# Performance work log

Measured on AMD Instinct MI355X. Metric: run time of the kernel, lower is better.

The kernel has to match this reference:

```python
import jax, jax.numpy as jnp
import numpy as np

F = 256  # filters
FQ = F // 8  # query/key channels


def setup_inputs() -> dict:
    key = jax.random.key(0)
    ks = jax.random.split(key, 9)
    B, H, W = 4, 64, 64
    s_in = 1.0 / np.sqrt(F)
    inp = {
        "inputs": jax.random.normal(ks[0], (B, H, W, F), jnp.float32),
        "Wq": jax.random.normal(ks[1], (F, FQ), jnp.float32) * s_in,
        "bq": jnp.zeros((FQ,), jnp.float32),
        "Wk": jax.random.normal(ks[2], (F, FQ), jnp.float32) * s_in,
        "bk": jnp.zeros((FQ,), jnp.float32),
        "Wv": jax.random.normal(ks[3], (F, F), jnp.float32) * s_in,
        "bv": jnp.zeros((F,), jnp.float32),
        "Wo": jax.random.normal(ks[4], (F, F), jnp.float32) * s_in,
        "bo": jnp.zeros((F,), jnp.float32),
    }
    return inp


def reference(inputs, Wq, bq, Wk, bk, Wv, bv, Wo, bo):
    B, H, W, C = inputs.shape
    N = H * W
    x = inputs.reshape(B, N, C)  # 1x1 conv == per-token linear
    q = jax.nn.relu(jnp.einsum('bnc,cd->bnd', x, Wq) + bq)  # [B,N,FQ]
    k = jax.nn.relu(jnp.einsum('bnc,cd->bnd', x, Wk) + bk)  # [B,N,FQ]
    v = jax.nn.relu(jnp.einsum('bnc,cd->bnd', x, Wv) + bv)  # [B,N,C]
    # unscaled full attention (as in the original module)
    attn = jax.nn.softmax(jnp.einsum('bnd,bmd->bnm', q, k), axis=-1)  # [B,N,N]
    attended = jnp.einsum('bnm,bmc->bnc', attn, v)  # [B,N,C]
    out = jax.nn.relu(jnp.einsum('bnc,cd->bnd', attended, Wo) + bo)
    return inputs + out.reshape(B, H, W, C)
```

## Files before the change

kernel.cpp:

```cpp
#include <hip/hip_runtime.h>

typedef __attribute__((ext_vector_type(8))) short short8;
typedef __attribute__((ext_vector_type(4))) float floatx4;

#define MFMA16(a, b, c) __builtin_amdgcn_mfma_f32_16x16x32_bf16((a), (b), (c), 0, 0, 0)

#define LDP 72
#define LDO 264
#define LOG2E 1.4426950408889634f
#define PSHIFT 23.083120654223414f

__device__ __forceinline__ float bf2f(unsigned short u) {
  return __uint_as_float(((unsigned int)u) << 16);
}
__device__ __forceinline__ unsigned short f2bf(float f) {
  unsigned int x = __float_as_uint(f);
  x += 0x7FFFu + ((x >> 16) & 1u);
  return (unsigned short)(x >> 16);
}
__device__ __forceinline__ float ld_in(const void* p, long i, int isf32) {
  if (isf32) return ((const float*)p)[i];
  return bf2f(((const unsigned short*)p)[i]);
}
__device__ __forceinline__ short8 ld16(const unsigned short* p) {
  return *(const short8*)__builtin_assume_aligned(p, 16);
}
__device__ __forceinline__ void st16(unsigned short* p, short8 v) {
  *(short8*)__builtin_assume_aligned(p, 16) = v;
}
__device__ __forceinline__ int detect_bad(const unsigned short* x, int idx) {
  const short8 v = ld16(x + (long)idx * 8);
  int bad = 0;
#pragma unroll
  for (int j = 0; j < 8; j++) {
    const unsigned int e = (((unsigned short)v[j]) >> 7) & 0xFFu;
    if (e >= 141u) bad = 1;
  }
  return bad;
}


__global__ __launch_bounds__(256)
void proj_kernel(const void* __restrict__ x,
                 const void* __restrict__ Wq, const void* __restrict__ bq,
                 const void* __restrict__ Wk, const void* __restrict__ bk,
                 const void* __restrict__ Wv, const void* __restrict__ bv,
                 const void* __restrict__ Wo,
                 unsigned short* __restrict__ Qf, unsigned short* __restrict__ Kf,
                 unsigned short* __restrict__ Vf, unsigned short* __restrict__ Wf_o) {
  __shared__ unsigned short Wl[64][LDO];
  __shared__ unsigned short Vl[64][LDP];
  __shared__ int flagl[4];
  const int t = (int)threadIdx.x;
  const int wave = t >> 6, lane = t & 63, quad = lane >> 4, l15 = lane & 15;

  {
    const int bad = detect_bad((const unsigned short*)x, t) |
                    detect_bad((const unsigned short*)x, 256 + t);
    if (lane == 0) flagl[wave] = (__ballot(bad) != 0ull) ? 1 : 0;
  }
  __syncthreads();
  const int isf32 = flagl[0] | flagl[1] | flagl[2] | flagl[3];

  const int blk = (int)blockIdx.x;
  if (blk >= 1280) {
    const int b2 = blk - 1280;
    const int g0 = (b2 >> 2) * 64, c0 = (b2 & 3) * 64;
    const int j = t & 63, r4 = t >> 6;
#pragma unroll
    for (int k2 = 0; k2 < 16; k2++) {
      const int rr = r4 * 16 + k2;
      Vl[j][rr] = f2bf(ld_in(Wo, (long)(c0 + rr) * 256 + g0 + j, isf32));
    }
    __syncthreads();
#pragma unroll
    for (int cc = 0; cc < 2; cc++) {
      const int c = t + cc * 256;
      const int f_l = c >> 6, lane_c = c & 63;
      const int og = f_l >> 1, kse = f_l & 1;
      const int out_l = lane_c & 15, q = lane_c >> 4;
      const short8 v = ld16(&Vl[og * 16 + out_l][kse * 32 + q * 8]);
      st16(Wf_o + (long)(((g0 >> 4) + og) * 8 + (c0 >> 5) + kse) * 512 + lane_c * 8, v);
    }
    return;
  }

  const int ct = blk % 5;
  const long row_base = (long)(blk / 5) * 64;

  if (ct == 0) {
    for (int i = t; i < 16384; i += 256) {
      const int g = i & 63, c = i >> 6;
      const float v = (g < 32) ? ld_in(Wq, (long)c * 32 + g, isf32) * LOG2E
                               : ld_in(Wk, (long)c * 32 + (g - 32), isf32);
      Wl[g][c] = f2bf(v);
    }
  } else {
    const int g0 = (ct - 1) * 64;
    for (int i = t; i < 16384; i += 256) {
      const int j = i & 63, c = i >> 6;
      Wl[j][c] = f2bf(ld_in(Wv, (long)c * 256 + g0 + j, isf32));
    }
  }
  __syncthreads();

  const long arow = row_base + wave * 16 + l15;
  floatx4 acc[4];
  acc[0] = acc[1] = acc[2] = acc[3] = (floatx4)0.0f;

#pragma unroll
  for (int ks = 0; ks < 8; ks++) {
    short8 a;
    if (isf32) {
      const float* xf = (const float*)x + arow * 256 + ks * 32 + quad * 8;
      floatx4 f0 = *(const floatx4*)xf;
      floatx4 f1 = *(const floatx4*)(xf + 4);
#pragma unroll
      for (int j = 0; j < 4; j++) { a[j] = (short)f2bf(f0[j]); a[4 + j] = (short)f2bf(f1[j]); }
    } else {
      a = ld16((const unsigned short*)x + arow * 256 + ks * 32 + quad * 8);
    }
#pragma unroll
    for (int tn = 0; tn < 4; tn++) {
      const short8 bfr = ld16(&Wl[tn * 16 + l15][ks * 32 + quad * 8]);
      acc[tn] = MFMA16(a, bfr, acc[tn]);
    }
  }

  if (ct == 0) {
#pragma unroll
    for (int tn = 0; tn < 4; tn++) {
      const int g = tn * 16 + l15;
      const float bias = (g < 32) ? ld_in(bq, g, isf32) * LOG2E
                                  : ld_in(bk, g - 32, isf32);
#pragma unroll
      for (int r = 0; r < 4; r++)
        Vl[wave * 16 + quad * 4 + r][g] = f2bf(fmaxf(acc[tn][r] + bias, 0.0f));
    }
    __syncthreads();
    const long f0 = row_base >> 4;
#pragma unroll
    for (int cc = 0; cc < 2; cc++) {
      const int c = t + cc * 256;
      const int isK = c >> 8;
      const int c2 = c & 255;
      const int f_l = c2 >> 6, lane_c = c2 & 63;
      const int row_l = lane_c & 15, q = lane_c >> 4;
      const short8 v = ld16(&Vl[f_l * 16 + row_l][isK * 32 + q * 8]);
      unsigned short* dst = isK ? Kf : Qf;
      st16(dst + (f0 + f_l) * 512 + lane_c * 8, v);
    }
  } else {
#pragma unroll
    for (int tn = 0; tn < 4; tn++) {
      const float bias = ld_in(bv, (long)(ct - 1) * 64 + tn * 16 + l15, isf32);
#pragma unroll
      for (int r = 0; r < 4; r++)
        Vl[tn * 16 + l15][wave * 16 + quad * 4 + r] =
            f2bf(fmaxf(acc[tn][r] + bias, 0.0f));
    }
    __syncthreads();
    const long bb = row_base >> 12;
    const int kt = (int)((row_base & 4095) >> 6);
    const long fbase = (bb * 64 + kt) * 32 + (long)(ct - 1) * 8;
#pragma unroll
    for (int cc = 0; cc < 2; cc++) {
      const int c = t * 2 + cc;
      const int f_l = c >> 6, lane_c = c & 63;
      const int cg = f_l >> 1, kh = f_l & 1;
      const int ch_l = lane_c & 15, q = lane_c >> 4;
      const short8 v = ld16(&Vl[cg * 16 + ch_l][kh * 32 + q * 8]);
      st16(Vf + (fbase + f_l) * 512 + lane_c * 8, v);
    }
  }
}

__global__ __launch_bounds__(512, 2)
void flash_kernel(const unsigned short* __restrict__ Qf,
                  const unsigned short* __restrict__ Kf,
                  const unsigned short* __restrict__ Vf,
                  const unsigned short* __restrict__ Wf_o,
                  const void* __restrict__ bo,
                  const void* __restrict__ xin, void* __restrict__ out) {
  __shared__ unsigned short Pl[2][64 * LDP];
  __shared__ unsigned short Ol[64 * LDO];
  __shared__ float Lp[2][64];
  __shared__ float Ll[64];
  __shared__ int flagl[8];

  const int t = (int)threadIdx.x;
  const int wave = t >> 6, lane = t & 63, quad = lane >> 4, l15 = lane & 15;

  {
    const int bad = detect_bad((const unsigned short*)xin, t);
    if (lane == 0) flagl[wave] = (__ballot(bad) != 0ull) ? 1 : 0;
  }

  const int raw = (int)blockIdx.x;
  const int b = raw & 3;
  const int mt = raw >> 2;
  const long qrow0 = (long)b * 4096 + (long)mt * 64;
  const int m = wave & 3, h = wave >> 2;

  const long kfrag0 = (long)b * 256;
  const long vfrag0 = (long)b * 64 * 32;

  const short8 qf = ld16(Qf + ((qrow0 >> 4) + m) * 512 + lane * 8);
  short8 kb[2];
#pragma unroll
  for (int i = 0; i < 2; i++)
    kb[i] = ld16(Kf + (kfrag0 + h * 2 + i) * 512 + lane * 8);

  floatx4 oacc[4][2];
#pragma unroll
  for (int i = 0; i < 4; i++) { oacc[i][0] = (floatx4)0.0f; oacc[i][1] = (floatx4)0.0f; }
  float lpart[4] = {0.0f, 0.0f, 0.0f, 0.0f};

  for (int kt = 0; kt < 64; kt++) {
    short8 vb[2][2];
#pragma unroll
    for (int tv = 0; tv < 2; tv++)
#pragma unroll
      for (int kh = 0; kh < 2; kh++)
        vb[tv][kh] = ld16(Vf + (vfrag0 + (long)kt * 32 + (wave * 2 + tv) * 2 + kh) * 512 + lane * 8);

    floatx4 s[2];
#pragma unroll
    for (int i = 0; i < 2; i++) { s[i] = (floatx4)0.0f; s[i] = MFMA16(qf, kb[i], s[i]); }
    const int ktn = (kt + 1) & 63;
#pragma unroll
    for (int i = 0; i < 2; i++)
      kb[i] = ld16(Kf + (kfrag0 + ktn * 4 + h * 2 + i) * 512 + lane * 8);

    unsigned short* pl = Pl[kt & 1];
#pragma unroll
    for (int i = 0; i < 2; i++)
#pragma unroll
      for (int r = 0; r < 4; r++) {
        const float p = exp2f(s[i][r] - PSHIFT);
        lpart[r] += p;
        pl[(m * 16 + quad * 4 + r) * LDP + h * 32 + i * 16 + l15] = f2bf(p);
      }
    __syncthreads();

    const unsigned short* plr = Pl[kt & 1];
    short8 pa[4][2];
#pragma unroll
    for (int rm = 0; rm < 4; rm++)
#pragma unroll
      for (int kh = 0; kh < 2; kh++)
        pa[rm][kh] = ld16(&plr[(rm * 16 + l15) * LDP + kh * 32 + quad * 8]);

#pragma unroll
    for (int kh = 0; kh < 2; kh++)
#pragma unroll
      for (int tv = 0; tv < 2; tv++)
#pragma unroll
        for (int rm = 0; rm < 4; rm++)
          oacc[rm][tv] = MFMA16(pa[rm][kh], vb[tv][kh], oacc[rm][tv]);
  }

#pragma unroll
  for (int r = 0; r < 4; r++)
#pragma unroll
    for (int off = 1; off < 16; off <<= 1)
      lpart[r] += __shfl_xor(lpart[r], off);
  if (l15 == 0) {
    floatx4 lw;
#pragma unroll
    for (int r = 0; r < 4; r++) lw[r] = lpart[r];
    *(floatx4*)&Lp[h][m * 16 + quad * 4] = lw;
  }
  __syncthreads();
  if (t < 64) Ll[t] = 1.0f / (Lp[0][t] + Lp[1][t]);
  __syncthreads();

#pragma unroll
  for (int rm = 0; rm < 4; rm++) {
    const floatx4 ll = *(const floatx4*)&Ll[rm * 16 + quad * 4];
#pragma unroll
    for (int tv = 0; tv < 2; tv++)
#pragma unroll
      for (int r = 0; r < 4; r++)
        Ol[(rm * 16 + quad * 4 + r) * LDO + wave * 32 + tv * 16 + l15] =
            f2bf(oacc[rm][tv][r] * ll[r]);
  }
  __syncthreads();

  const int isf32 = flagl[0] | flagl[1] | flagl[2] | flagl[3] |
                    flagl[4] | flagl[5] | flagl[6] | flagl[7];
  const int m2 = wave & 3, gh = wave >> 2;
  floatx4 acc2[8];
#pragma unroll
  for (int i = 0; i < 8; i++) acc2[i] = (floatx4)0.0f;
#pragma unroll
  for (int ks = 0; ks < 8; ks++) {
    const short8 a = ld16(&Ol[(m2 * 16 + l15) * LDO + ks * 32 + quad * 8]);
#pragma unroll
    for (int tn = 0; tn < 8; tn++) {
      const short8 bfr = ld16(Wf_o + (long)((gh * 8 + tn) * 8 + ks) * 512 + lane * 8);
      acc2[tn] = MFMA16(a, bfr, acc2[tn]);
    }
  }
  __syncthreads();
#pragma unroll
  for (int tn = 0; tn < 8; tn++) {
    const int g = gh * 128 + tn * 16 + l15;
    const float bias = ld_in(bo, g, isf32);
#pragma unroll
    for (int r = 0; r < 4; r++)
      Ol[(m2 * 16 + quad * 4 + r) * LDO + g] = f2bf(fmaxf(acc2[tn][r] + bias, 0.0f));
  }
  __syncthreads();

  if (isf32) {
    const float* xf = (const float*)xin + qrow0 * 256;
    float* of = (float*)out + qrow0 * 256;
#pragma unroll
    for (int p = 0; p < 8; p++) {
      const int idx = p * 2048 + t * 4;
      const int row = idx >> 8, ch = idx & 255;
      floatx4 xv = *(const floatx4*)(xf + idx);
      floatx4 ov;
#pragma unroll
      for (int j = 0; j < 4; j++) ov[j] = bf2f(Ol[row * LDO + ch + j]) + xv[j];
      *(floatx4*)(of + idx) = ov;
    }
  } else {
    const unsigned short* xh = (const unsigned short*)xin + qrow0 * 256;
    unsigned short* oh = (unsigned short*)out + qrow0 * 256;
#pragma unroll
    for (int p = 0; p < 4; p++) {
      const int idx = p * 4096 + t * 8;
      const int row = idx >> 8, ch = idx & 255;
      const short8 xv = ld16(xh + idx);
      short8 ov;
#pragma unroll
      for (int j = 0; j < 8; j++)
        ov[j] = (short)f2bf(bf2f(Ol[row * LDO + ch + j]) + bf2f((unsigned short)xv[j]));
      st16(oh + idx, ov);
    }
  }
}

extern "C" void kernel_launch(void* const* d_in, const int* in_sizes, int n_in,
                              void* d_out, int out_size, void* d_ws, size_t ws_size,
                              hipStream_t stream) {
  const void* x  = d_in[0];
  const void* Wq = d_in[1]; const void* bq = d_in[2];
  const void* Wk = d_in[3]; const void* bk = d_in[4];
  const void* Wv = d_in[5]; const void* bv = d_in[6];
  const void* Wo = d_in[7]; const void* bo = d_in[8];

  char* ws = (char*)d_ws;
  unsigned short* Qf   = (unsigned short*)ws;
  unsigned short* Kf   = Qf + (long)4 * 4096 * 32;
  unsigned short* Vf   = Kf + (long)4 * 4096 * 32;
  unsigned short* Wf_o = Vf + (long)4 * 256 * 4096;

  proj_kernel<<<1296, 256, 0, stream>>>(x, Wq, bq, Wk, bk, Wv, bv, Wo,
                                        Qf, Kf, Vf, Wf_o);
  flash_kernel<<<256, 512, 0, stream>>>(Qf, Kf, Vf, Wf_o, bo, x, d_out);
}
```

Baseline: 203.4 us.

## Fuse projection and flash attention into one cooperative kernel with grid sync

Merges the projection kernel and the flash-attention kernel into a single cooperative launch of 256 blocks. Each block projects its own 64 rows (Q/K and four V chunks) while holding the input fragments in registers, and the first 16 blocks also repack Wo; a grid-wide sync then separates this phase from attention. The attention loop is unrolled to handle two key tiles per iteration with a larger double-buffered P tile, which halves the barriers. This removes one kernel launch and its gap, in exchange for more LDS per block, a grid-sync cost, every block reloading the full Wv weights, and a projection phase with far fewer blocks than before.

```diff
diff --git a/kernel.cpp b/kernel.cpp
--- a/kernel.cpp
+++ b/kernel.cpp
@@ -1,4 +1,7 @@
 #include <hip/hip_runtime.h>
+#include <hip/hip_cooperative_groups.h>
+
+namespace cg = cooperative_groups;
 
 typedef __attribute__((ext_vector_type(8))) short short8;
 typedef __attribute__((ext_vector_type(4))) float floatx4;
@@ -40,224 +43,212 @@
 }
 
 
-__global__ __launch_bounds__(256)
-void proj_kernel(const void* __restrict__ x,
-                 const void* __restrict__ Wq, const void* __restrict__ bq,
-                 const void* __restrict__ Wk, const void* __restrict__ bk,
-                 const void* __restrict__ Wv, const void* __restrict__ bv,
-                 const void* __restrict__ Wo,
-                 unsigned short* __restrict__ Qf, unsigned short* __restrict__ Kf,
-                 unsigned short* __restrict__ Vf, unsigned short* __restrict__ Wf_o) {
+__global__ __launch_bounds__(512, 2)
+void fused_kernel(const void* __restrict__ x,
+                  const void* __restrict__ Wq, const void* __restrict__ bq,
+                  const void* __restrict__ Wk, const void* __restrict__ bk,
+                  const void* __restrict__ Wv, const void* __restrict__ bv,
+                  const void* __restrict__ Wo, const void* __restrict__ bo,
+                  unsigned short* __restrict__ Qf, unsigned short* __restrict__ Kf,
+                  unsigned short* __restrict__ Vf, unsigned short* __restrict__ Wf_o,
+                  void* __restrict__ out) {
   __shared__ unsigned short Wl[64][LDO];
   __shared__ unsigned short Vl[64][LDP];
-  __shared__ int flagl[4];
+  __shared__ unsigned short Pl[2][2][64 * LDP];
+  __shared__ unsigned short Ol[64 * LDO];
+  __shared__ float Lp[2][64];
+  __shared__ float Ll[64];
+  __shared__ int flagl[8];
+
   const int t = (int)threadIdx.x;
   const int wave = t >> 6, lane = t & 63, quad = lane >> 4, l15 = lane & 15;
 
   {
-    const int bad = detect_bad((const unsigned short*)x, t) |
-                    detect_bad((const unsigned short*)x, 256 + t);
+    const int bad = detect_bad((const unsigned short*)x, t);
     if (lane == 0) flagl[wave] = (__ballot(bad) != 0ull) ? 1 : 0;
   }
   __syncthreads();
-  const int isf32 = flagl[0] | flagl[1] | flagl[2] | flagl[3];
-
-  const int blk = (int)blockIdx.x;
-  if (blk >= 1280) {
-    const int b2 = blk - 1280;
-    const int g0 = (b2 >> 2) * 64, c0 = (b2 & 3) * 64;
-    const int j = t & 63, r4 = t >> 6;
-#pragma unroll
-    for (int k2 = 0; k2 < 16; k2++) {
-      const int rr = r4 * 16 + k2;
-      Vl[j][rr] = f2bf(ld_in(Wo, (long)(c0 + rr) * 256 + g0 + j, isf32));
-    }
-    __syncthreads();
-#pragma unroll
-    for (int cc = 0; cc < 2; cc++) {
-      const int c = t + cc * 256;
-      const int f_l = c >> 6, lane_c = c & 63;
+  const int isf32 = flagl[0] | flagl[1] | flagl[2] | flagl[3] |
+                    flagl[4] | flagl[5] | flagl[6] | flagl[7];
+
+  const int raw = (int)blockIdx.x;
+  const int b = raw & 3;
+  const int mt = raw >> 2;
+  const long row_base = (long)b * 4096 + (long)mt * 64;
+
+  const int pm = wave & 3, ph = wave >> 2;
+  {
+    const long arow = row_base + pm * 16 + l15;
+    short8 a[8];
+#pragma unroll
+    for (int ks = 0; ks < 8; ks++) {
+      if (isf32) {
+        const float* xf = (const float*)x + arow * 256 + ks * 32 + quad * 8;
+        floatx4 f0 = *(const floatx4*)xf;
+        floatx4 f1 = *(const floatx4*)(xf + 4);
+#pragma unroll
+        for (int j = 0; j < 4; j++) { a[ks][j] = (short)f2bf(f0[j]); a[ks][4 + j] = (short)f2bf(f1[j]); }
+      } else {
+        a[ks] = ld16((const unsigned short*)x + arow * 256 + ks * 32 + quad * 8);
+      }
+    }
+
+    for (int chunk = 0; chunk < 5; chunk++) {
+      __syncthreads();
+      if (chunk == 0) {
+        for (int i = t; i < 16384; i += 512) {
+          const int g = i & 63, c = i >> 6;
+          const float v = (g < 32) ? ld_in(Wq, (long)c * 32 + g, isf32) * LOG2E
+                                   : ld_in(Wk, (long)c * 32 + (g - 32), isf32);
+          Wl[g][c] = f2bf(v);
+        }
+      } else {
+        const int g0 = (chunk - 1) * 64;
+        for (int i = t; i < 16384; i += 512) {
+          const int j = i & 63, c = i >> 6;
+          Wl[j][c] = f2bf(ld_in(Wv, (long)c * 256 + g0 + j, isf32));
+        }
+      }
+      __syncthreads();
+
+      floatx4 acc[2];
+      acc[0] = acc[1] = (floatx4)0.0f;
+#pragma unroll
+      for (int ks = 0; ks < 8; ks++)
+#pragma unroll
+        for (int tn = 0; tn < 2; tn++) {
+          const short8 bfr = ld16(&Wl[ph * 32 + tn * 16 + l15][ks * 32 + quad * 8]);
+          acc[tn] = MFMA16(a[ks], bfr, acc[tn]);
+        }
+
+      if (chunk == 0) {
+#pragma unroll
+        for (int tn = 0; tn < 2; tn++) {
+          const int g = ph * 32 + tn * 16 + l15;
+          const float bias = (g < 32) ? ld_in(bq, g, isf32) * LOG2E
+                                      : ld_in(bk, g - 32, isf32);
+#pragma unroll
+          for (int r = 0; r < 4; r++)
+            Vl[pm * 16 + quad * 4 + r][g] = f2bf(fmaxf(acc[tn][r] + bias, 0.0f));
+        }
+        __syncthreads();
+        const int isK = t >> 8, c2 = t & 255;
+        const int f_l = c2 >> 6, lane_c = c2 & 63;
+        const int row_l = lane_c & 15, q = lane_c >> 4;
+        const short8 v = ld16(&Vl[f_l * 16 + row_l][isK * 32 + q * 8]);
+        unsigned short* dst = isK ? Kf : Qf;
+        st16(dst + ((row_base >> 4) + f_l) * 512 + lane_c * 8, v);
+      } else {
+        const int vc = chunk - 1;
+#pragma unroll
+        for (int tn = 0; tn < 2; tn++) {
+          const float bias = ld_in(bv, (long)vc * 64 + ph * 32 + tn * 16 + l15, isf32);
+#pragma unroll
+          for (int r = 0; r < 4; r++)
+            Vl[ph * 32 + tn * 16 + l15][pm * 16 + quad * 4 + r] =
+                f2bf(fmaxf(acc[tn][r] + bias, 0.0f));
+        }
+        __syncthreads();
+        const int f_l = t >> 6, lane_c = t & 63;
+        const int cg2 = f_l >> 1, kh = f_l & 1;
+        const int ch_l = lane_c & 15, q = lane_c >> 4;
+        const short8 v = ld16(&Vl[cg2 * 16 + ch_l][kh * 32 + q * 8]);
+        const long fbase = ((long)b * 64 + mt) * 32 + (long)vc * 8;
+        st16(Vf + (fbase + f_l) * 512 + lane_c * 8, v);
+      }
+    }
+
+    if (raw < 16) {
+      __syncthreads();
+      const int g0 = (raw >> 2) * 64, c0 = (raw & 3) * 64;
+      const int j = t & 63, r8 = t >> 6;
+#pragma unroll
+      for (int k2 = 0; k2 < 8; k2++) {
+        const int rr = r8 * 8 + k2;
+        Vl[j][rr] = f2bf(ld_in(Wo, (long)(c0 + rr) * 256 + g0 + j, isf32));
+      }
+      __syncthreads();
+      const int f_l = t >> 6, lane_c = t & 63;
       const int og = f_l >> 1, kse = f_l & 1;
       const int out_l = lane_c & 15, q = lane_c >> 4;
       const short8 v = ld16(&Vl[og * 16 + out_l][kse * 32 + q * 8]);
       st16(Wf_o + (long)(((g0 >> 4) + og) * 8 + (c0 >> 5) + kse) * 512 + lane_c * 8, v);
     }
-    return;
-  }
-
-  const int ct = blk % 5;
-  const long row_base = (long)(blk / 5) * 64;
-
-  if (ct == 0) {
-    for (int i = t; i < 16384; i += 256) {
-      const int g = i & 63, c = i >> 6;
-      const float v = (g < 32) ? ld_in(Wq, (long)c * 32 + g, isf32) * LOG2E
-                               : ld_in(Wk, (long)c * 32 + (g - 32), isf32);
-      Wl[g][c] = f2bf(v);
-    }
-  } else {
-    const int g0 = (ct - 1) * 64;
-    for (int i = t; i < 16384; i += 256) {
-      const int j = i & 63, c = i >> 6;
-      Wl[j][c] = f2bf(ld_in(Wv, (long)c * 256 + g0 + j, isf32));
-    }
-  }
-  __syncthreads();
-
-  const long arow = row_base + wave * 16 + l15;
-  floatx4 acc[4];
-  acc[0] = acc[1] = acc[2] = acc[3] = (floatx4)0.0f;
-
-#pragma unroll
-  for (int ks = 0; ks < 8; ks++) {
-    short8 a;
-    if (isf32) {
-      const float* xf = (const float*)x + arow * 256 + ks * 32 + quad * 8;
-      floatx4 f0 = *(const floatx4*)xf;
-      floatx4 f1 = *(const floatx4*)(xf + 4);
-#pragma unroll
-      for (int j = 0; j < 4; j++) { a[j] = (short)f2bf(f0[j]); a[4 + j] = (short)f2bf(f1[j]); }
-    } else {
-      a = ld16((const unsigned short*)x + arow * 256 + ks * 32 + quad * 8);
-    }
-#pragma unroll
-    for (int tn = 0; tn < 4; tn++) {
-      const short8 bfr = ld16(&Wl[tn * 16 + l15][ks * 32 + quad * 8]);
-      acc[tn] = MFMA16(a, bfr, acc[tn]);
-    }
-  }
-
-  if (ct == 0) {
-#pragma unroll
-    for (int tn = 0; tn < 4; tn++) {
-      const int g = tn * 16 + l15;
-      const float bias = (g < 32) ? ld_in(bq, g, isf32) * LOG2E
-                                  : ld_in(bk, g - 32, isf32);
-#pragma unroll
-      for (int r = 0; r < 4; r++)
-        Vl[wave * 16 + quad * 4 + r][g] = f2bf(fmaxf(acc[tn][r] + bias, 0.0f));
-    }
-    __syncthreads();
-    const long f0 = row_base >> 4;
-#pragma unroll
-    for (int cc = 0; cc < 2; cc++) {
-      const int c = t + cc * 256;
-      const int isK = c >> 8;
-      const int c2 = c & 255;
-      const int f_l = c2 >> 6, lane_c = c2 & 63;
-      const int row_l = lane_c & 15, q = lane_c >> 4;
-      const short8 v = ld16(&Vl[f_l * 16 + row_l][isK * 32 + q * 8]);
-      unsigned short* dst = isK ? Kf : Qf;
-      st16(dst + (f0 + f_l) * 512 + lane_c * 8, v);
-    }
-  } else {
-#pragma unroll
-    for (int tn = 0; tn < 4; tn++) {
-      const float bias = ld_in(bv, (long)(ct - 1) * 64 + tn * 16 + l15, isf32);
-#pragma unroll
-      for (int r = 0; r < 4; r++)
-        Vl[tn * 16 + l15][wave * 16 + quad * 4 + r] =
-            f2bf(fmaxf(acc[tn][r] + bias, 0.0f));
-    }
-    __syncthreads();
-    const long bb = row_base >> 12;
-    const int kt = (int)((row_base & 4095) >> 6);
-    const long fbase = (bb * 64 + kt) * 32 + (long)(ct - 1) * 8;
-#pragma unroll
-    for (int cc = 0; cc < 2; cc++) {
-      const int c = t * 2 + cc;
-      const int f_l = c >> 6, lane_c = c & 63;
-      const int cg = f_l >> 1, kh = f_l & 1;
-      const int ch_l = lane_c & 15, q = lane_c >> 4;
-      const short8 v = ld16(&Vl[cg * 16 + ch_l][kh * 32 + q * 8]);
-      st16(Vf + (fbase + f_l) * 512 + lane_c * 8, v);
-    }
-  }
-}
-
-__global__ __launch_bounds__(512, 2)
-void flash_kernel(const unsigned short* __restrict__ Qf,
-                  const unsigned short* __restrict__ Kf,
-                  const unsigned short* __restrict__ Vf,
-                  const unsigned short* __restrict__ Wf_o,
-                  const void* __restrict__ bo,
-                  const void* __restrict__ xin, void* __restrict__ out) {
-  __shared__ unsigned short Pl[2][64 * LDP];
-  __shared__ unsigned short Ol[64 * LDO];
-  __shared__ float Lp[2][64];
-  __shared__ float Ll[64];
-  __shared__ int flagl[8];
-
-  const int t = (int)threadIdx.x;
-  const int wave = t >> 6, lane = t & 63, quad = lane >> 4, l15 = lane & 15;
-
-  {
-    const int bad = detect_bad((const unsigned short*)xin, t);
-    if (lane == 0) flagl[wave] = (__ballot(bad) != 0ull) ? 1 : 0;
-  }
-
-  const int raw = (int)blockIdx.x;
-  const int b = raw & 3;
-  const int mt = raw >> 2;
-  const long qrow0 = (long)b * 4096 + (long)mt * 64;
+  }
+
+  cg::this_grid().sync();
+
+  const long qrow0 = row_base;
   const int m = wave & 3, h = wave >> 2;
-
   const long kfrag0 = (long)b * 256;
-  const long vfrag0 = (long)b * 64 * 32;
+  const long vfrag0 = (long)b * 2048;
 
   const short8 qf = ld16(Qf + ((qrow0 >> 4) + m) * 512 + lane * 8);
-  short8 kb[2];
-#pragma unroll
-  for (int i = 0; i < 2; i++)
-    kb[i] = ld16(Kf + (kfrag0 + h * 2 + i) * 512 + lane * 8);
+  short8 kb[2][2];
+#pragma unroll
+  for (int tt = 0; tt < 2; tt++)
+#pragma unroll
+    for (int i = 0; i < 2; i++)
+      kb[tt][i] = ld16(Kf + (kfrag0 + tt * 4 + h * 2 + i) * 512 + lane * 8);
 
   floatx4 oacc[4][2];
 #pragma unroll
   for (int i = 0; i < 4; i++) { oacc[i][0] = (floatx4)0.0f; oacc[i][1] = (floatx4)0.0f; }
   float lpart[4] = {0.0f, 0.0f, 0.0f, 0.0f};
 
-  for (int kt = 0; kt < 64; kt++) {
-    short8 vb[2][2];
-#pragma unroll
-    for (int tv = 0; tv < 2; tv++)
+  for (int it = 0; it < 32; it++) {
+    const int kt0 = it * 2;
+    short8 vb[2][2][2];
+#pragma unroll
+    for (int tt = 0; tt < 2; tt++)
+#pragma unroll
+      for (int tv = 0; tv < 2; tv++)
+#pragma unroll
+        for (int kh = 0; kh < 2; kh++)
+          vb[tt][tv][kh] = ld16(Vf + (vfrag0 + (long)(kt0 + tt) * 32 + (wave * 2 + tv) * 2 + kh) * 512 + lane * 8);
+
+    floatx4 s[2][2];
+#pragma unroll
+    for (int tt = 0; tt < 2; tt++)
+#pragma unroll
+      for (int i = 0; i < 2; i++) { s[tt][i] = (floatx4)0.0f; s[tt][i] = MFMA16(qf, kb[tt][i], s[tt][i]); }
+#pragma unroll
+    for (int tt = 0; tt < 2; tt++)
+#pragma unroll
+      for (int i = 0; i < 2; i++)
+        kb[tt][i] = ld16(Kf + (kfrag0 + (long)((kt0 + 2 + tt) & 63) * 4 + h * 2 + i) * 512 + lane * 8);
+
+#pragma unroll
+    for (int tt = 0; tt < 2; tt++) {
+      unsigned short* pl = Pl[it & 1][tt];
+#pragma unroll
+      for (int i = 0; i < 2; i++)
+#pragma unroll
+        for (int r = 0; r < 4; r++) {
+          const float p = exp2f(s[tt][i][r] - PSHIFT);
+          lpart[r] += p;
+          pl[(m * 16 + quad * 4 + r) * LDP + h * 32 + i * 16 + l15] = f2bf(p);
+        }
+    }
+    __syncthreads();
+
+#pragma unroll
+    for (int tt = 0; tt < 2; tt++) {
+      const unsigned short* plr = Pl[it & 1][tt];
+      short8 pa[4][2];
+#pragma unroll
+      for (int rm = 0; rm < 4; rm++)
+#pragma unroll
+        for (int kh = 0; kh < 2; kh++)
+          pa[rm][kh] = ld16(&plr[(rm * 16 + l15) * LDP + kh * 32 + quad * 8]);
 #pragma unroll
       for (int kh = 0; kh < 2; kh++)
-        vb[tv][kh] = ld16(Vf + (vfrag0 + (long)kt * 32 + (wave * 2 + tv) * 2 + kh) * 512 + lane * 8);
-
-    floatx4 s[2];
-#pragma unroll
-    for (int i = 0; i < 2; i++) { s[i] = (floatx4)0.0f; s[i] = MFMA16(qf, kb[i], s[i]); }
-    const int ktn = (kt + 1) & 63;
-#pragma unroll
-    for (int i = 0; i < 2; i++)
-      kb[i] = ld16(Kf + (kfrag0 + ktn * 4 + h * 2 + i) * 512 + lane * 8);
-
-    unsigned short* pl = Pl[kt & 1];
-#pragma unroll
-    for (int i = 0; i < 2; i++)
-#pragma unroll
-      for (int r = 0; r < 4; r++) {
-        const float p = exp2f(s[i][r] - PSHIFT);
-        lpart[r] += p;
-        pl[(m * 16 + quad * 4 + r) * LDP + h * 32 + i * 16 + l15] = f2bf(p);
-      }
-    __syncthreads();
-
-    const unsigned short* plr = Pl[kt & 1];
-    short8 pa[4][2];
-#pragma unroll
-    for (int rm = 0; rm < 4; rm++)
-#pragma unroll
-      for (int kh = 0; kh < 2; kh++)
-        pa[rm][kh] = ld16(&plr[(rm * 16 + l15) * LDP + kh * 32 + quad * 8]);
-
-#pragma unroll
-    for (int kh = 0; kh < 2; kh++)
-#pragma unroll
-      for (int tv = 0; tv < 2; tv++)
-#pragma unroll
-        for (int rm = 0; rm < 4; rm++)
-          oacc[rm][tv] = MFMA16(pa[rm][kh], vb[tv][kh], oacc[rm][tv]);
+#pragma unroll
+        for (int tv = 0; tv < 2; tv++)
+#pragma unroll
+          for (int rm = 0; rm < 4; rm++)
+            oacc[rm][tv] = MFMA16(pa[rm][kh], vb[tt][tv][kh], oacc[rm][tv]);
+    }
   }
 
 #pragma unroll
@@ -287,8 +278,6 @@
   }
   __syncthreads();
 
-  const int isf32 = flagl[0] | flagl[1] | flagl[2] | flagl[3] |
-                    flagl[4] | flagl[5] | flagl[6] | flagl[7];
   const int m2 = wave & 3, gh = wave >> 2;
   floatx4 acc2[8];
 #pragma unroll
@@ -314,7 +303,7 @@
   __syncthreads();
 
   if (isf32) {
-    const float* xf = (const float*)xin + qrow0 * 256;
+    const float* xf = (const float*)x + qrow0 * 256;
     float* of = (float*)out + qrow0 * 256;
 #pragma unroll
     for (int p = 0; p < 8; p++) {
@@ -327,7 +316,7 @@
       *(floatx4*)(of + idx) = ov;
     }
   } else {
-    const unsigned short* xh = (const unsigned short*)xin + qrow0 * 256;
+    const unsigned short* xh = (const unsigned short*)x + qrow0 * 256;
     unsigned short* oh = (unsigned short*)out + qrow0 * 256;
 #pragma unroll
     for (int p = 0; p < 4; p++) {
@@ -357,8 +346,11 @@
   unsigned short* Kf   = Qf + (long)4 * 4096 * 32;
   unsigned short* Vf   = Kf + (long)4 * 4096 * 32;
   unsigned short* Wf_o = Vf + (long)4 * 256 * 4096;
-
-  proj_kernel<<<1296, 256, 0, stream>>>(x, Wq, bq, Wk, bk, Wv, bv, Wo,
-                                        Qf, Kf, Vf, Wf_o);
-  flash_kernel<<<256, 512, 0, stream>>>(Qf, Kf, Vf, Wf_o, bo, x, d_out);
-}
+  void* out = d_out;
+
+  void* kargs[] = {(void*)&x, (void*)&Wq, (void*)&bq, (void*)&Wk, (void*)&bk,
+                   (void*)&Wv, (void*)&bv, (void*)&Wo, (void*)&bo,
+                   (void*)&Qf, (void*)&Kf, (void*)&Vf, (void*)&Wf_o, (void*)&out};
+  hipLaunchCooperativeKernel((const void*)fused_kernel, dim3(256), dim3(512),
+                             kargs, 0, stream);
+}
```

After: 232.6 us. 14.4% more time.
